# Kernel optimization log

Hardware: AMD Instinct MI355X
Metric: run time of the kernel (lower is better)

Reference implementation:

```python
import jax, jax.numpy as jnp
import numpy as np

B, SQ, SK = 2, 2048, 2048   # batch, n_query, n_memory
D, H, DFF = 1024, 16, 1024  # model dim, heads, ffn dim (must equal D per source constraints)
DH = D // H                 # head dim = 64
NEG = 1e9


def _split_heads(x):
    # (B, S, D) -> (B, H, S, DH)
    b, s, _ = x.shape
    return x.reshape(b, s, H, DH).transpose(0, 2, 1, 3)


def setup_inputs() -> dict:
    key = jax.random.key(0)
    ks = jax.random.split(key, 10)
    s = 0.02
    return {
        "q": jax.random.normal(ks[0], (B, SQ, D), jnp.float32),
        "k": jax.random.normal(ks[1], (B, SK, D), jnp.float32),
        "v": jax.random.normal(ks[2], (B, SK, D), jnp.float32),
        "Win_w": jax.random.normal(ks[3], (DFF, D), jnp.float32) * s,
        "Win_b": jnp.zeros((DFF,), jnp.float32),
        "Wff_w": jax.random.normal(ks[4], (D, DFF), jnp.float32) * s,
        "Wff_b": jnp.zeros((D,), jnp.float32),
        "Wout_w": jax.random.normal(ks[5], (D, D), jnp.float32) * s,
        "Wout_b": jnp.zeros((D,), jnp.float32),
        "attn_mask": jax.random.randint(ks[6], (B, SK), 0, 2, jnp.int32),
    }


def reference(q, k, v, Win_w, Win_b, Wff_w, Wff_b, Wout_w, Wout_b, attn_mask):
    # projections (in_linear; k,v additionally pass through out_linear as in source)
    qh = q @ Win_w.T + Win_b
    kh = (k @ Win_w.T + Win_b) @ Wout_w.T + Wout_b
    vh = (v @ Win_w.T + Win_b) @ Wout_w.T + Wout_b
    qh = qh * (D ** -0.5)

    qh, kh, vh = _split_heads(qh), _split_heads(kh), _split_heads(vh)

    # additive mask bias: 0 where mask==1, -1e9 where mask==0, broadcast over heads/queries
    bias = (attn_mask.astype(jnp.float32) - 1.0) * NEG  # (B, SK)
    scores = jnp.einsum("bhqd,bhkd->bhqk", qh, kh) + bias[:, None, None, :]
    probs = jax.nn.softmax(scores, axis=-1)
    out = jnp.einsum("bhqk,bhkd->bhqd", probs, vh)

    # merge heads: (B, H, SQ, DH) -> (B, SQ, D)
    out = out.transpose(0, 2, 1, 3).reshape(B, SQ, D)

    out = out @ Wff_w.T + Wff_b
    out = out @ Wout_w.T + Wout_b
    return out
```

## Files before the change

kernel.cpp:

```cpp
#include <hip/hip_runtime.h>
#include <hip/hip_bf16.h>
#include <cstdint>
#include <cstddef>

using u16 = unsigned short;
using u32 = unsigned int;

typedef __attribute__((ext_vector_type(8))) short short8;
typedef __attribute__((ext_vector_type(4))) float f32x4;

#define MFMA16(a, b, c) __builtin_amdgcn_mfma_f32_16x16x32_bf16((a), (b), (c), 0, 0, 0)

#define QSCALE 0.0450842200f

__device__ __forceinline__ u16 f2bf(float f) {
  u32 u = __float_as_uint(f);
  return (u16)((u + 0x7FFFu + ((u >> 16) & 1u)) >> 16);
}

__device__ __forceinline__ u32 pack_bf16(float a, float b) {
  u32 r;
  asm("v_cvt_pk_bf16_f32 %0, %1, %2" : "=v"(r) : "v"(a), "v"(b));
  return r;
}

__device__ __forceinline__ void gload_lds16(const u16* g, u16* l) {
  __builtin_amdgcn_global_load_lds((const __attribute__((address_space(1))) void*)g,
                                   (__attribute__((address_space(3))) void*)l, 16, 0, 0);
}

__global__ __launch_bounds__(256) void cvt_f32_bf16(const float* __restrict__ in,
                                                    u16* __restrict__ out, int n4) {
  int i = blockIdx.x * 256 + threadIdx.x;
  if (i >= n4) return;
  float4 v = reinterpret_cast<const float4*>(in)[i];
  u32 lo = (u32)f2bf(v.x) | ((u32)f2bf(v.y) << 16);
  u32 hi = (u32)f2bf(v.z) | ((u32)f2bf(v.w) << 16);
  reinterpret_cast<uint2*>(out)[i] = make_uint2(lo, hi);
}

__global__ __launch_bounds__(256) void cvt_qkv(const float* __restrict__ q,
                                               const float* __restrict__ k,
                                               const float* __restrict__ v,
                                               u16* __restrict__ X) {
  int i4 = blockIdx.x * 256 + threadIdx.x;
  const float* src = (i4 < 1048576) ? q : (i4 < 2097152) ? k : v;
  int loc = i4 & 1048575;
  float4 w = reinterpret_cast<const float4*>(src)[loc];
  u32 lo = (u32)f2bf(w.x) | ((u32)f2bf(w.y) << 16);
  u32 hi = (u32)f2bf(w.z) | ((u32)f2bf(w.w) << 16);
  reinterpret_cast<uint2*>(X)[i4] = make_uint2(lo, hi);
}

__global__ __launch_bounds__(256) void trans2(const float* __restrict__ in0,
                                              const float* __restrict__ in1,
                                              u16* __restrict__ out0,
                                              u16* __restrict__ out1) {
  const float* in = blockIdx.z ? in1 : in0;
  u16* out = blockIdx.z ? out1 : out0;
  __shared__ float tile[64][68];
  const int t = threadIdx.x;
  const int bx = blockIdx.x * 64, by = blockIdx.y * 64;
  const int r = t >> 2, c16 = (t & 3) * 16;
#pragma unroll
  for (int i = 0; i < 4; ++i)
    *reinterpret_cast<float4*>(&tile[r][c16 + i * 4]) =
        *reinterpret_cast<const float4*>(&in[(size_t)(bx + r) * 1024 + by + c16 + i * 4]);
  __syncthreads();
  const int jj = t >> 2, i16 = (t & 3) * 16;
#pragma unroll
  for (int i = 0; i < 4; ++i) {
    uint2 p;
    p.x = (u32)f2bf(tile[i16 + i * 4 + 0][jj]) | ((u32)f2bf(tile[i16 + i * 4 + 1][jj]) << 16);
    p.y = (u32)f2bf(tile[i16 + i * 4 + 2][jj]) | ((u32)f2bf(tile[i16 + i * 4 + 3][jj]) << 16);
    *reinterpret_cast<uint2*>(&out[(size_t)(by + jj) * 1024 + bx + i16 + i * 4]) = p;
  }
}

__global__ __launch_bounds__(256) void bias_comb(const float* __restrict__ W,
                                                 const float* __restrict__ bin,
                                                 const float* __restrict__ badd,
                                                 float* __restrict__ outb) {
  const int w = threadIdx.x >> 6, l = threadIdx.x & 63;
  const int j = blockIdx.x * 4 + w;
  const float4* Wr = reinterpret_cast<const float4*>(W + (size_t)j * 1024);
  const float4* br = reinterpret_cast<const float4*>(bin);
  float s = 0.f;
  for (int i = l; i < 256; i += 64) {
    float4 a = Wr[i], b = br[i];
    s += a.x * b.x + a.y * b.y + a.z * b.z + a.w * b.w;
  }
#pragma unroll
  for (int o = 1; o < 64; o <<= 1) s += __shfl_xor(s, o);
  if (l == 0) outb[j] = s + badd[j];
}

__global__ __launch_bounds__(256) void gemm_w2(const u16* __restrict__ A,
                                               const u16* __restrict__ Bt0,
                                               const u16* __restrict__ Bt1,
                                               u16* __restrict__ C0,
                                               u16* __restrict__ C1) {
  const u16* Bt = blockIdx.z ? Bt1 : Bt0;
  u16* C = blockIdx.z ? C1 : C0;
  __shared__ __align__(16) u16 As[64 * 64];
  __shared__ __align__(16) u16 Bs[64 * 64];
  const int t = threadIdx.x, w = t >> 6, l = t & 63;
  const int l15 = l & 15, l4 = l >> 4;
  const int m0 = blockIdx.x * 64, n0 = blockIdx.y * 64;
  f32x4 acc[4] = {};
  const int row0 = t >> 3, cs0 = t & 7;
  const int c0 = cs0 ^ (row0 & 7);
  const int row1 = row0 + 32;
  const int c1 = cs0 ^ (row1 & 7);
  const u16* gA0 = A + (size_t)(m0 + row0) * 1024 + c0 * 8;
  const u16* gA1 = A + (size_t)(m0 + row1) * 1024 + c1 * 8;
  const u16* gB0 = Bt + (size_t)(n0 + row0) * 1024 + c0 * 8;
  const u16* gB1 = Bt + (size_t)(n0 + row1) * 1024 + c1 * 8;
  u16* lA0 = As + w * 512;
  u16* lA1 = As + 2048 + w * 512;
  u16* lB0 = Bs + w * 512;
  u16* lB1 = Bs + 2048 + w * 512;
  for (int k0 = 0; k0 < 1024; k0 += 64) {
    __syncthreads();
    gload_lds16(gA0 + k0, lA0);
    gload_lds16(gA1 + k0, lA1);
    gload_lds16(gB0 + k0, lB0);
    gload_lds16(gB1 + k0, lB1);
    __syncthreads();
#pragma unroll
    for (int ks = 0; ks < 2; ++ks) {
      const int cc = ks * 4 + l4;
      short8 bfr = *reinterpret_cast<const short8*>(&Bs[(w * 16 + l15) * 64 + ((cc ^ (l15 & 7)) * 8)]);
#pragma unroll
      for (int i = 0; i < 4; ++i) {
        short8 afr = *reinterpret_cast<const short8*>(&As[(i * 16 + l15) * 64 + ((cc ^ (l15 & 7)) * 8)]);
        acc[i] = MFMA16(afr, bfr, acc[i]);
      }
    }
  }
#pragma unroll
  for (int i = 0; i < 4; ++i)
#pragma unroll
    for (int j = 0; j < 4; ++j)
      C[(size_t)(m0 + i * 16 + l4 * 4 + j) * 1024 + n0 + w * 16 + l15] = f2bf(acc[i][j]);
}

__global__ __launch_bounds__(256) void proj(const u16* __restrict__ X,
                                            const u16* __restrict__ Winb,
                                            const u16* __restrict__ Wc2,
                                            const float* __restrict__ Win_b,
                                            const float* __restrict__ bias2,
                                            u16* __restrict__ Qh,
                                            u16* __restrict__ Kp,
                                            u16* __restrict__ VT) {
  __shared__ __align__(16) u16 As[128 * 32];
  __shared__ __align__(16) u16 Bs[128 * 32];
  const int t = threadIdx.x, w = t >> 6, l = t & 63;
  const int l15 = l & 15, l4 = l >> 4;
  const int seg = blockIdx.x >> 5;
  const int m0 = blockIdx.x * 128;
  const int n0 = blockIdx.y * 128;
  const int wr = (w >> 1) * 64, wc = (w & 1) * 64;
  const u16* Bt = seg == 0 ? Winb : Wc2;
  const float* bias = seg == 0 ? Win_b : bias2;

  f32x4 acc[4][4] = {};
  const u16* gA = X + (size_t)(m0 + (t >> 2)) * 1024 + (t & 3) * 8;
  const u16* gB = Bt + (size_t)(n0 + (t >> 2)) * 1024 + (t & 3) * 8;
  u16* lA = &As[0] + w * 512;
  u16* lB = &Bs[0] + w * 512;

  for (int k0 = 0; k0 < 1024; k0 += 32) {
    __syncthreads();
    gload_lds16(gA, lA);
    gload_lds16(gA + 64 * 1024, lA + 2048);
    gload_lds16(gB, lB);
    gload_lds16(gB + 64 * 1024, lB + 2048);
    gA += 32;
    gB += 32;
    __syncthreads();
    short8 af[4], bf[4];
#pragma unroll
    for (int i = 0; i < 4; ++i)
      af[i] = *reinterpret_cast<const short8*>(&As[(wr + i * 16 + l15) * 32 + l4 * 8]);
#pragma unroll
    for (int i = 0; i < 4; ++i)
      bf[i] = *reinterpret_cast<const short8*>(&Bs[(wc + i * 16 + l15) * 32 + l4 * 8]);
#pragma unroll
    for (int mi = 0; mi < 4; ++mi)
#pragma unroll
      for (int ni = 0; ni < 4; ++ni)
        acc[mi][ni] = MFMA16(af[mi], bf[ni], acc[mi][ni]);
  }

#pragma unroll
  for (int mi = 0; mi < 4; ++mi) {
#pragma unroll
    for (int ni = 0; ni < 4; ++ni) {
      const int col = n0 + wc + ni * 16 + l15;
      const float bv = bias[col];
      const int row0 = m0 + wr + mi * 16 + l4 * 4;
      if (seg == 0) {
#pragma unroll
        for (int j = 0; j < 4; ++j)
          Qh[(size_t)(row0 + j) * 1024 + col] = f2bf((acc[mi][ni][j] + bv) * QSCALE);
      } else if (seg == 1) {
#pragma unroll
        for (int j = 0; j < 4; ++j)
          Kp[(size_t)(row0 - 4096 + j) * 1024 + col] = f2bf(acc[mi][ni][j] + bv);
      } else {
        const int r = row0 - 8192;
        const int bb = r >> 11;
        const int sk = r & 2047;
        u32 p0 = (u32)f2bf(acc[mi][ni][0] + bv) | ((u32)f2bf(acc[mi][ni][1] + bv) << 16);
        u32 p1 = (u32)f2bf(acc[mi][ni][2] + bv) | ((u32)f2bf(acc[mi][ni][3] + bv) << 16);
        *reinterpret_cast<uint2*>(VT + ((size_t)(bb * 1024 + col)) * 2048 + sk) = make_uint2(p0, p1);
      }
    }
  }
}

__global__ __launch_bounds__(512) void attn(const u16* __restrict__ Qh,
                                            const u16* __restrict__ Kb,
                                            const u16* __restrict__ VT,
                                            const int* __restrict__ mask,
                                            u16* __restrict__ AO) {
  __shared__ __align__(16) u16 Kt[64 * 64];
  __shared__ __align__(16) u16 Vt[64 * 64];
  __shared__ __align__(16) u16 Pw[8 * 16 * 64];
  __shared__ float biasS[2048];
  const int t = threadIdx.x, l = t & 63, w = t >> 6;
  const int l15 = l & 15, l4 = l >> 4;
  const int q0 = blockIdx.x * 128;
  const int bh = blockIdx.y, b = bh >> 4, h = bh & 15;

  for (int i = t; i < 2048; i += 512) biasS[i] = mask[b * 2048 + i] ? 0.f : -1.442695e9f;

  short8 qf[2];
  {
    const u16* qp = Qh + (size_t)(b * 2048 + q0 + w * 16 + l15) * 1024 + h * 64 + l4 * 8;
    qf[0] = *reinterpret_cast<const short8*>(qp);
    qf[1] = *reinterpret_cast<const short8*>(qp + 32);
  }
  short8 ones;
#pragma unroll
  for (int i = 0; i < 8; ++i) ones[i] = (short)0x3F80;

  f32x4 acc[4] = {};
  f32x4 accS = {};

  const int rr = t >> 3, cs = t & 7;
  const int ck = cs ^ (rr & 7);
  const u16* gK = Kb + (size_t)(b * 2048 + rr) * 1024 + h * 64 + ck * 8;
  u16* ldsK = Kt + w * 512;
  const u32* gV = reinterpret_cast<const u32*>(VT) + (size_t)(b * 1024 + h * 64 + rr) * 1024 + ck;
  const int pws = w * 1024;

  for (int kt = 0; kt < 2048; kt += 64) {
    const u32* gvt = gV + (kt >> 1);
    u32 A0 = gvt[0], A1 = gvt[8], A2 = gvt[16], A3 = gvt[24];
    __syncthreads();
    gload_lds16(gK + (size_t)kt * 1024, ldsK);
    uint4 vv;
    vv.x = (A0 & 0xffffu) | (A1 << 16);
    vv.y = (A2 & 0xffffu) | (A3 << 16);
    vv.z = (A0 >> 16) | (A1 & 0xffff0000u);
    vv.w = (A2 >> 16) | (A3 & 0xffff0000u);
    *reinterpret_cast<uint4*>(&Vt[rr * 64 + cs * 8]) = vv;
    __syncthreads();

    f32x4 s[4] = {};
#pragma unroll
    for (int ks = 0; ks < 2; ++ks) {
      const int cc = ks * 4 + l4;
#pragma unroll
      for (int n = 0; n < 4; ++n) {
        short8 kb = *reinterpret_cast<const short8*>(&Kt[(n * 16 + l15) * 64 + ((cc ^ (l15 & 7)) * 8)]);
        s[n] = MFMA16(qf[ks], kb, s[n]);
      }
    }
#pragma unroll
    for (int n = 0; n < 4; ++n) {
      const float bv = biasS[kt + n * 16 + l15];
#pragma unroll
      for (int j = 0; j < 4; ++j) s[n][j] = __builtin_amdgcn_exp2f(s[n][j] + bv);
    }
#pragma unroll
    for (int j = 0; j < 4; ++j) {
      const int r = l4 * 4 + j;
      uint2 pk;
      pk.x = pack_bf16(s[0][j], s[1][j]);
      pk.y = pack_bf16(s[2][j], s[3][j]);
      *reinterpret_cast<uint2*>(
          &Pw[pws + r * 64 + (((l15 >> 1) ^ (r & 7)) * 8) + (l15 & 1) * 4]) = pk;
    }
#pragma unroll
    for (int ks = 0; ks < 2; ++ks) {
      const int cc = ks * 4 + l4;
      short8 pa = *reinterpret_cast<const short8*>(&Pw[pws + l15 * 64 + ((cc ^ (l15 & 7)) * 8)]);
#pragma unroll
      for (int n = 0; n < 4; ++n) {
        short8 vb = *reinterpret_cast<const short8*>(&Vt[(n * 16 + l15) * 64 + ((cc ^ (l15 & 7)) * 8)]);
        acc[n] = MFMA16(pa, vb, acc[n]);
      }
      accS = MFMA16(pa, ones, accS);
    }
  }

  const size_t orow0 = (size_t)(b * 2048 + q0 + w * 16 + l4 * 4);
#pragma unroll
  for (int j = 0; j < 4; ++j) {
    const float inv = 1.0f / accS[j];
#pragma unroll
    for (int n = 0; n < 4; ++n)
      AO[(orow0 + j) * 1024 + h * 64 + n * 16 + l15] = f2bf(acc[n][j] * inv);
  }
}

__global__ __launch_bounds__(256) void gemm_tail(const u16* __restrict__ A,
                                                 const u16* __restrict__ Bt,
                                                 const float* __restrict__ bias,
                                                 float* __restrict__ C) {
  __shared__ __align__(16) u16 As[128 * 32];
  __shared__ __align__(16) u16 Bs[64 * 32];
  const int t = threadIdx.x, w = t >> 6, l = t & 63;
  const int l15 = l & 15, l4 = l >> 4;
  const int m0 = blockIdx.x * 128, n0 = blockIdx.y * 64;
  const int wr = (w >> 1) * 64, wc = (w & 1) * 32;
  f32x4 acc[4][2] = {};
  const u16* gA = A + (size_t)(m0 + (t >> 2)) * 1024 + (t & 3) * 8;
  const u16* gB = Bt + (size_t)(n0 + (t >> 2)) * 1024 + (t & 3) * 8;
  u16* lA = &As[0] + w * 512;
  u16* lB = &Bs[0] + w * 512;

  for (int k0 = 0; k0 < 1024; k0 += 32) {
    __syncthreads();
    gload_lds16(gA, lA);
    gload_lds16(gA + 64 * 1024, lA + 2048);
    gload_lds16(gB, lB);
    gA += 32;
    gB += 32;
    __syncthreads();
    short8 af[4], bf[2];
#pragma unroll
    for (int i = 0; i < 4; ++i)
      af[i] = *reinterpret_cast<const short8*>(&As[(wr + i * 16 + l15) * 32 + l4 * 8]);
#pragma unroll
    for (int i = 0; i < 2; ++i)
      bf[i] = *reinterpret_cast<const short8*>(&Bs[(wc + i * 16 + l15) * 32 + l4 * 8]);
#pragma unroll
    for (int mi = 0; mi < 4; ++mi)
#pragma unroll
      for (int ni = 0; ni < 2; ++ni)
        acc[mi][ni] = MFMA16(af[mi], bf[ni], acc[mi][ni]);
  }

#pragma unroll
  for (int mi = 0; mi < 4; ++mi) {
#pragma unroll
    for (int ni = 0; ni < 2; ++ni) {
      const int col = n0 + wc + ni * 16 + l15;
      const float bv = bias[col];
      const int row0 = m0 + wr + mi * 16 + l4 * 4;
#pragma unroll
      for (int j = 0; j < 4; ++j)
        C[(size_t)(row0 + j) * 1024 + col] = acc[mi][ni][j] + bv;
    }
  }
}

extern "C" void kernel_launch(void* const* d_in, const int* in_sizes, int n_in,
                              void* d_out, int out_size, void* d_ws, size_t ws_size,
                              hipStream_t stream) {
  const float* q = (const float*)d_in[0];
  const float* k = (const float*)d_in[1];
  const float* v = (const float*)d_in[2];
  const float* Win_w = (const float*)d_in[3];
  const float* Win_b = (const float*)d_in[4];
  const float* Wff_w = (const float*)d_in[5];
  const float* Wff_b = (const float*)d_in[6];
  const float* Wout_w = (const float*)d_in[7];
  const float* Wout_b = (const float*)d_in[8];
  const int* mask = (const int*)d_in[9];
  float* out = (float*)d_out;

  char* ws = (char*)d_ws;
  u16* Xbf = (u16*)ws;
  u16* AO = (u16*)ws;
  u16* Qh = (u16*)(ws + 25165824);
  u16* WinT = (u16*)(ws + 25165824);
  u16* Woutb = (u16*)(ws + 27262976);
  u16* WffT = (u16*)(ws + 29360128);
  u16* Kproj = (u16*)(ws + 33554432);
  u16* VT = (u16*)(ws + 41943040);
  u16* Wc2 = (u16*)(ws + 50331648);
  u16* Wc3 = (u16*)(ws + 52428800);
  u16* Winb = (u16*)(ws + 54525952);
  float* bias3 = (float*)(ws + 54525952);
  float* bias2 = out;

  bias_comb<<<256, 256, 0, stream>>>(Wout_w, Win_b, Wout_b, bias2);
  cvt_qkv<<<12288, 256, 0, stream>>>(q, k, v, Xbf);
  cvt_f32_bf16<<<1024, 256, 0, stream>>>(Wout_w, Woutb, 262144);
  cvt_f32_bf16<<<1024, 256, 0, stream>>>(Win_w, Winb, 262144);
  trans2<<<dim3(16, 16, 2), 256, 0, stream>>>(Win_w, Wff_w, WinT, WffT);
  gemm_w2<<<dim3(16, 16, 2), 256, 0, stream>>>(Woutb, WinT, WffT, Wc2, Wc3);
  proj<<<dim3(96, 8), 256, 0, stream>>>(Xbf, Winb, Wc2, Win_b, bias2, Qh, Kproj, VT);
  attn<<<dim3(16, 32), 512, 0, stream>>>(Qh, Kproj, VT, mask, AO);
  bias_comb<<<256, 256, 0, stream>>>(Wout_w, Wff_b, Wout_b, bias3);
  gemm_tail<<<dim3(32, 16), 256, 0, stream>>>(AO, Wc3, bias3, out);
}
```

Baseline: 162.2 us.

## Double-buffer LDS in GEMMs, merge weight prep kernels, fold Q scale into weights

Adds double-buffered LDS staging to gemm_w2, proj and gemm_tail, so the next k-tile's global-to-LDS loads are issued before the current tile's MFMAs and one barrier per iteration is dropped. Merges the two weight conversions and the transpose kernel into a single prep launch. Folds the query scale into Win_w and Win_b at prep time, removing the multiply from the projection epilogue. The trade-off is double the LDS use per block, which may lower occupancy, and the bf16 rounding of the pre-scaled weights differs slightly.

```diff
diff --git a/kernel.cpp b/kernel.cpp
--- a/kernel.cpp
+++ b/kernel.cpp
@@ -1,5 +1,4 @@
 #include <hip/hip_runtime.h>
-#include <hip/hip_bf16.h>
 #include <cstdint>
 #include <cstddef>
 
@@ -27,16 +26,6 @@
 __device__ __forceinline__ void gload_lds16(const u16* g, u16* l) {
   __builtin_amdgcn_global_load_lds((const __attribute__((address_space(1))) void*)g,
                                    (__attribute__((address_space(3))) void*)l, 16, 0, 0);
-}
-
-__global__ __launch_bounds__(256) void cvt_f32_bf16(const float* __restrict__ in,
-                                                    u16* __restrict__ out, int n4) {
-  int i = blockIdx.x * 256 + threadIdx.x;
-  if (i >= n4) return;
-  float4 v = reinterpret_cast<const float4*>(in)[i];
-  u32 lo = (u32)f2bf(v.x) | ((u32)f2bf(v.y) << 16);
-  u32 hi = (u32)f2bf(v.z) | ((u32)f2bf(v.w) << 16);
-  reinterpret_cast<uint2*>(out)[i] = make_uint2(lo, hi);
 }
 
 __global__ __launch_bounds__(256) void cvt_qkv(const float* __restrict__ q,
@@ -52,28 +41,48 @@
   reinterpret_cast<uint2*>(X)[i4] = make_uint2(lo, hi);
 }
 
-__global__ __launch_bounds__(256) void trans2(const float* __restrict__ in0,
-                                              const float* __restrict__ in1,
-                                              u16* __restrict__ out0,
-                                              u16* __restrict__ out1) {
-  const float* in = blockIdx.z ? in1 : in0;
-  u16* out = blockIdx.z ? out1 : out0;
+__global__ __launch_bounds__(256) void prep(const float* __restrict__ Wout_w,
+                                            const float* __restrict__ Win_w,
+                                            const float* __restrict__ Wff_w,
+                                            const float* __restrict__ Win_b,
+                                            u16* __restrict__ Woutb, u16* __restrict__ Winb,
+                                            u16* __restrict__ WinT, u16* __restrict__ WffT,
+                                            float* __restrict__ bias1f) {
   __shared__ float tile[64][68];
   const int t = threadIdx.x;
-  const int bx = blockIdx.x * 64, by = blockIdx.y * 64;
-  const int r = t >> 2, c16 = (t & 3) * 16;
-#pragma unroll
-  for (int i = 0; i < 4; ++i)
-    *reinterpret_cast<float4*>(&tile[r][c16 + i * 4]) =
-        *reinterpret_cast<const float4*>(&in[(size_t)(bx + r) * 1024 + by + c16 + i * 4]);
-  __syncthreads();
-  const int jj = t >> 2, i16 = (t & 3) * 16;
-#pragma unroll
-  for (int i = 0; i < 4; ++i) {
-    uint2 p;
-    p.x = (u32)f2bf(tile[i16 + i * 4 + 0][jj]) | ((u32)f2bf(tile[i16 + i * 4 + 1][jj]) << 16);
-    p.y = (u32)f2bf(tile[i16 + i * 4 + 2][jj]) | ((u32)f2bf(tile[i16 + i * 4 + 3][jj]) << 16);
-    *reinterpret_cast<uint2*>(&out[(size_t)(by + jj) * 1024 + bx + i16 + i * 4]) = p;
+  const int bid = blockIdx.x;
+  if (bid < 2048) {
+    const float* src = bid < 1024 ? Wout_w : Win_w;
+    u16* dst = bid < 1024 ? Woutb : Winb;
+    const float sc = bid < 1024 ? 1.0f : QSCALE;
+    int i = (bid & 1023) * 256 + t;
+    float4 v = reinterpret_cast<const float4*>(src)[i];
+    u32 lo = (u32)f2bf(v.x * sc) | ((u32)f2bf(v.y * sc) << 16);
+    u32 hi = (u32)f2bf(v.z * sc) | ((u32)f2bf(v.w * sc) << 16);
+    reinterpret_cast<uint2*>(dst)[i] = make_uint2(lo, hi);
+  } else if (bid < 2560) {
+    const float* in = bid < 2304 ? Win_w : Wff_w;
+    u16* out = bid < 2304 ? WinT : WffT;
+    const int tix = (bid - 2048) & 255;
+    const int bx = (tix >> 4) * 64, by = (tix & 15) * 64;
+    const int r = t >> 2, c16 = (t & 3) * 16;
+#pragma unroll
+    for (int i = 0; i < 4; ++i)
+      *reinterpret_cast<float4*>(&tile[r][c16 + i * 4]) =
+          *reinterpret_cast<const float4*>(&in[(size_t)(bx + r) * 1024 + by + c16 + i * 4]);
+    __syncthreads();
+    const int jj = t >> 2, i16 = (t & 3) * 16;
+#pragma unroll
+    for (int i = 0; i < 4; ++i) {
+      uint2 p;
+      p.x = (u32)f2bf(tile[i16 + i * 4 + 0][jj]) | ((u32)f2bf(tile[i16 + i * 4 + 1][jj]) << 16);
+      p.y = (u32)f2bf(tile[i16 + i * 4 + 2][jj]) | ((u32)f2bf(tile[i16 + i * 4 + 3][jj]) << 16);
+      *reinterpret_cast<uint2*>(&out[(size_t)(by + jj) * 1024 + bx + i16 + i * 4]) = p;
+    }
+  } else {
+    float4 v = reinterpret_cast<const float4*>(Win_b)[t];
+    v.x *= QSCALE; v.y *= QSCALE; v.z *= QSCALE; v.w *= QSCALE;
+    reinterpret_cast<float4*>(bias1f)[t] = v;
   }
 }
 
@@ -102,8 +111,8 @@
                                                u16* __restrict__ C1) {
   const u16* Bt = blockIdx.z ? Bt1 : Bt0;
   u16* C = blockIdx.z ? C1 : C0;
-  __shared__ __align__(16) u16 As[64 * 64];
-  __shared__ __align__(16) u16 Bs[64 * 64];
+  __shared__ __align__(16) u16 As[2][4096];
+  __shared__ __align__(16) u16 Bs[2][4096];
   const int t = threadIdx.x, w = t >> 6, l = t & 63;
   const int l15 = l & 15, l4 = l >> 4;
   const int m0 = blockIdx.x * 64, n0 = blockIdx.y * 64;
@@ -116,24 +125,23 @@
   const u16* gA1 = A + (size_t)(m0 + row1) * 1024 + c1 * 8;
   const u16* gB0 = Bt + (size_t)(n0 + row0) * 1024 + c0 * 8;
   const u16* gB1 = Bt + (size_t)(n0 + row1) * 1024 + c1 * 8;
-  u16* lA0 = As + w * 512;
-  u16* lA1 = As + 2048 + w * 512;
-  u16* lB0 = Bs + w * 512;
-  u16* lB1 = Bs + 2048 + w * 512;
-  for (int k0 = 0; k0 < 1024; k0 += 64) {
-    __syncthreads();
-    gload_lds16(gA0 + k0, lA0);
-    gload_lds16(gA1 + k0, lA1);
-    gload_lds16(gB0 + k0, lB0);
-    gload_lds16(gB1 + k0, lB1);
-    __syncthreads();
+#define W2_STAGE(KK, DST)                             \
+  gload_lds16(gA0 + (KK), &As[DST][0] + w * 512);     \
+  gload_lds16(gA1 + (KK), &As[DST][2048] + w * 512);  \
+  gload_lds16(gB0 + (KK), &Bs[DST][0] + w * 512);     \
+  gload_lds16(gB1 + (KK), &Bs[DST][2048] + w * 512);
+  W2_STAGE(0, 0)
+  for (int step = 0; step < 16; ++step) {
+    const int c = step & 1;
+    __syncthreads();
+    if (step < 15) { W2_STAGE((step + 1) * 64, c ^ 1) }
 #pragma unroll
     for (int ks = 0; ks < 2; ++ks) {
       const int cc = ks * 4 + l4;
-      short8 bfr = *reinterpret_cast<const short8*>(&Bs[(w * 16 + l15) * 64 + ((cc ^ (l15 & 7)) * 8)]);
+      short8 bfr = *reinterpret_cast<const short8*>(&Bs[c][(w * 16 + l15) * 64 + ((cc ^ (l15 & 7)) * 8)]);
 #pragma unroll
       for (int i = 0; i < 4; ++i) {
-        short8 afr = *reinterpret_cast<const short8*>(&As[(i * 16 + l15) * 64 + ((cc ^ (l15 & 7)) * 8)]);
+        short8 afr = *reinterpret_cast<const short8*>(&As[c][(i * 16 + l15) * 64 + ((cc ^ (l15 & 7)) * 8)]);
         acc[i] = MFMA16(afr, bfr, acc[i]);
       }
     }
@@ -148,13 +156,13 @@
 __global__ __launch_bounds__(256) void proj(const u16* __restrict__ X,
                                             const u16* __restrict__ Winb,
                                             const u16* __restrict__ Wc2,
-                                            const float* __restrict__ Win_b,
+                                            const float* __restrict__ bias1f,
                                             const float* __restrict__ bias2,
                                             u16* __restrict__ Qh,
                                             u16* __restrict__ Kp,
                                             u16* __restrict__ VT) {
-  __shared__ __align__(16) u16 As[128 * 32];
-  __shared__ __align__(16) u16 Bs[128 * 32];
+  __shared__ __align__(16) u16 As[2][4096];
+  __shared__ __align__(16) u16 Bs[2][4096];
   const int t = threadIdx.x, w = t >> 6, l = t & 63;
   const int l15 = l & 15, l4 = l >> 4;
   const int seg = blockIdx.x >> 5;
@@ -162,30 +170,28 @@
   const int n0 = blockIdx.y * 128;
   const int wr = (w >> 1) * 64, wc = (w & 1) * 64;
   const u16* Bt = seg == 0 ? Winb : Wc2;
-  const float* bias = seg == 0 ? Win_b : bias2;
+  const float* bias = seg == 0 ? bias1f : bias2;
 
   f32x4 acc[4][4] = {};
   const u16* gA = X + (size_t)(m0 + (t >> 2)) * 1024 + (t & 3) * 8;
   const u16* gB = Bt + (size_t)(n0 + (t >> 2)) * 1024 + (t & 3) * 8;
-  u16* lA = &As[0] + w * 512;
-  u16* lB = &Bs[0] + w * 512;
-
-  for (int k0 = 0; k0 < 1024; k0 += 32) {
-    __syncthreads();
-    gload_lds16(gA, lA);
-    gload_lds16(gA + 64 * 1024, lA + 2048);
-    gload_lds16(gB, lB);
-    gload_lds16(gB + 64 * 1024, lB + 2048);
-    gA += 32;
-    gB += 32;
-    __syncthreads();
+#define PJ_STAGE(KK, DST)                                   \
+  gload_lds16(gA + (KK), &As[DST][0] + w * 512);            \
+  gload_lds16(gA + (KK) + 65536, &As[DST][2048] + w * 512); \
+  gload_lds16(gB + (KK), &Bs[DST][0] + w * 512);            \
+  gload_lds16(gB + (KK) + 65536, &Bs[DST][2048] + w * 512);
+  PJ_STAGE(0, 0)
+  for (int step = 0; step < 32; ++step) {
+    const int c = step & 1;
+    __syncthreads();
+    if (step < 31) { PJ_STAGE((step + 1) * 32, c ^ 1) }
     short8 af[4], bf[4];
 #pragma unroll
     for (int i = 0; i < 4; ++i)
-      af[i] = *reinterpret_cast<const short8*>(&As[(wr + i * 16 + l15) * 32 + l4 * 8]);
+      af[i] = *reinterpret_cast<const short8*>(&As[c][(wr + i * 16 + l15) * 32 + l4 * 8]);
 #pragma unroll
     for (int i = 0; i < 4; ++i)
-      bf[i] = *reinterpret_cast<const short8*>(&Bs[(wc + i * 16 + l15) * 32 + l4 * 8]);
+      bf[i] = *reinterpret_cast<const short8*>(&Bs[c][(wc + i * 16 + l15) * 32 + l4 * 8]);
 #pragma unroll
     for (int mi = 0; mi < 4; ++mi)
 #pragma unroll
@@ -203,7 +209,7 @@
       if (seg == 0) {
 #pragma unroll
         for (int j = 0; j < 4; ++j)
-          Qh[(size_t)(row0 + j) * 1024 + col] = f2bf((acc[mi][ni][j] + bv) * QSCALE);
+          Qh[(size_t)(row0 + j) * 1024 + col] = f2bf(acc[mi][ni][j] + bv);
       } else if (seg == 1) {
 #pragma unroll
         for (int j = 0; j < 4; ++j)
@@ -321,8 +327,8 @@
                                                  const u16* __restrict__ Bt,
                                                  const float* __restrict__ bias,
                                                  float* __restrict__ C) {
-  __shared__ __align__(16) u16 As[128 * 32];
-  __shared__ __align__(16) u16 Bs[64 * 32];
+  __shared__ __align__(16) u16 As[2][4096];
+  __shared__ __align__(16) u16 Bs[2][2048];
   const int t = threadIdx.x, w = t >> 6, l = t & 63;
   const int l15 = l & 15, l4 = l >> 4;
   const int m0 = blockIdx.x * 128, n0 = blockIdx.y * 64;
@@ -330,31 +336,28 @@
   f32x4 acc[4][2] = {};
   const u16* gA = A + (size_t)(m0 + (t >> 2)) * 1024 + (t & 3) * 8;
   const u16* gB = Bt + (size_t)(n0 + (t >> 2)) * 1024 + (t & 3) * 8;
-  u16* lA = &As[0] + w * 512;
-  u16* lB = &Bs[0] + w * 512;
-
-  for (int k0 = 0; k0 < 1024; k0 += 32) {
-    __syncthreads();
-    gload_lds16(gA, lA);
-    gload_lds16(gA + 64 * 1024, lA + 2048);
-    gload_lds16(gB, lB);
-    gA += 32;
-    gB += 32;
-    __syncthreads();
+#define TL_STAGE(KK, DST)                                   \
+  gload_lds16(gA + (KK), &As[DST][0] + w * 512);            \
+  gload_lds16(gA + (KK) + 65536, &As[DST][2048] + w * 512); \
+  gload_lds16(gB + (KK), &Bs[DST][0] + w * 512);
+  TL_STAGE(0, 0)
+  for (int step = 0; step < 32; ++step) {
+    const int c = step & 1;
+    __syncthreads();
+    if (step < 31) { TL_STAGE((step + 1) * 32, c ^ 1) }
     short8 af[4], bf[2];
 #pragma unroll
     for (int i = 0; i < 4; ++i)
-      af[i] = *reinterpret_cast<const short8*>(&As[(wr + i * 16 + l15) * 32 + l4 * 8]);
+      af[i] = *reinterpret_cast<const short8*>(&As[c][(wr + i * 16 + l15) * 32 + l4 * 8]);
 #pragma unroll
     for (int i = 0; i < 2; ++i)
-      bf[i] = *reinterpret_cast<const short8*>(&Bs[(wc + i * 16 + l15) * 32 + l4 * 8]);
+      bf[i] = *reinterpret_cast<const short8*>(&Bs[c][(wc + i * 16 + l15) * 32 + l4 * 8]);
 #pragma unroll
     for (int mi = 0; mi < 4; ++mi)
 #pragma unroll
       for (int ni = 0; ni < 2; ++ni)
         acc[mi][ni] = MFMA16(af[mi], bf[ni], acc[mi][ni]);
   }
-
 #pragma unroll
   for (int mi = 0; mi < 4; ++mi) {
 #pragma unroll
@@ -387,6 +390,7 @@
   char* ws = (char*)d_ws;
   u16* Xbf = (u16*)ws;
   u16* AO = (u16*)ws;
+  float* bias3 = (float*)(ws + 20971520);
   u16* Qh = (u16*)(ws + 25165824);
   u16* WinT = (u16*)(ws + 25165824);
   u16* Woutb = (u16*)(ws + 27262976);
@@ -396,17 +400,15 @@
   u16* Wc2 = (u16*)(ws + 50331648);
   u16* Wc3 = (u16*)(ws + 52428800);
   u16* Winb = (u16*)(ws + 54525952);
-  float* bias3 = (float*)(ws + 54525952);
   float* bias2 = out;
-
+  float* bias1f = out + 1024;
+
+  prep<<<2561, 256, 0, stream>>>(Wout_w, Win_w, Wff_w, Win_b, Woutb, Winb, WinT, WffT, bias1f);
+  cvt_qkv<<<12288, 256, 0, stream>>>(q, k, v, Xbf);
   bias_comb<<<256, 256, 0, stream>>>(Wout_w, Win_b, Wout_b, bias2);
-  cvt_qkv<<<12288, 256, 0, stream>>>(q, k, v, Xbf);
-  cvt_f32_bf16<<<1024, 256, 0, stream>>>(Wout_w, Woutb, 262144);
-  cvt_f32_bf16<<<1024, 256, 0, stream>>>(Win_w, Winb, 262144);
-  trans2<<<dim3(16, 16, 2), 256, 0, stream>>>(Win_w, Wff_w, WinT, WffT);
   gemm_w2<<<dim3(16, 16, 2), 256, 0, stream>>>(Woutb, WinT, WffT, Wc2, Wc3);
-  proj<<<dim3(96, 8), 256, 0, stream>>>(Xbf, Winb, Wc2, Win_b, bias2, Qh, Kproj, VT);
+  proj<<<dim3(96, 8), 256, 0, stream>>>(Xbf, Winb, Wc2, bias1f, bias2, Qh, Kproj, VT);
+  bias_comb<<<256, 256, 0, stream>>>(Wout_w, Wff_b, Wout_b, bias3);
   attn<<<dim3(16, 32), 512, 0, stream>>>(Qh, Kproj, VT, mask, AO);
-  bias_comb<<<256, 256, 0, stream>>>(Wout_w, Wff_b, Wout_b, bias3);
   gemm_tail<<<dim3(32, 16), 256, 0, stream>>>(AO, Wc3, bias3, out);
 }
```

Result: no change. 160.3 us (-1.2%).
